# Kernel tuning notes

Hardware: AMD Instinct MI355X
Metric: run time of the kernel (lower is better)

The kernel has to match this reference:

```python
import jax, jax.numpy as jnp
import numpy as np
import math

EMBED_DIMS = 256
NUM_LANDMARKS = 40  # hard-coded k=40 in the original module
B, N = 2, 8192


def setup_inputs() -> dict:
    key = jax.random.key(0)
    ks = jax.random.split(key, 9)
    C = EMBED_DIMS
    w = lambda k: jax.random.normal(k, (C, C), dtype=jnp.float32) * 0.02
    b = lambda k: jax.random.normal(k, (C,), dtype=jnp.float32) * 0.02
    return {
        "query": jax.random.normal(ks[0], (B, N, C), dtype=jnp.float32),
        "Wq": w(ks[1]), "bq": b(ks[2]),
        "Wk": w(ks[3]), "bk": b(ks[4]),
        "Wv": w(ks[5]), "bv": b(ks[6]),
        "Wo": w(ks[7]), "bo": b(ks[8]),
    }


def reference(query, Wq, bq, Wk, bk, Wv, bv, Wo, bo):
    # key = value = identity = query (defaults in the original forward)
    C = query.shape[-1]
    scaling = math.sqrt(C)

    q = query @ Wq.T + bq  # [B, N, C]
    k = query @ Wk.T + bk
    v = query @ Wv.T + bv

    # Full similarity only to score keys: score_m[b, m] = sum_n sim_nm[b, n, m]
    sim_nm = jnp.einsum('bnc,bmc->bnm', q, k) / scaling  # [B, N, N]
    score_m = sim_nm.sum(axis=1)                          # [B, N]

    _, top_idx = jax.lax.top_k(score_m, NUM_LANDMARKS)    # [B, 40]
    selected = jnp.take_along_axis(k, top_idx[:, :, None], axis=1)  # [B, 40, C]

    sim_qn = jax.nn.softmax(jnp.einsum('bnc,bkc->bnk', q, selected) / scaling, axis=-1)  # [B, N, 40]
    sim_km = jax.nn.softmax(jnp.einsum('bmc,bkc->bmk', k, selected) / scaling, axis=-1)  # [B, N, 40]

    sim_qk = jnp.einsum('bnk,bmk->bnm', sim_qn, sim_km)   # [B, N, N]
    out = jnp.einsum('bnm,bmc->bnc', sim_qk, v)           # [B, N, C]
    out = out @ Wo.T + bo
    return query + out  # identity residual; dropouts are identity at p=0
```

## Files before the change

### kernel.cpp

```cpp
#include <hip/hip_runtime.h>
#include <cstddef>
#include <cstdint>

#define BATCH 2
#define SEQ 8192
#define CH 256
#define NLM 40
#define MROWS (BATCH * SEQ)
#define INV_SCALE 0.0625f
#define NCBLK 256

typedef unsigned short ushort_t;
typedef __attribute__((ext_vector_type(8))) short short8;
typedef __attribute__((ext_vector_type(4))) float floatx4;

__device__ __forceinline__ ushort_t f2bf(float f) {
    unsigned int u = __float_as_uint(f);
    u += 0x7FFFu + ((u >> 16) & 1u);
    return (ushort_t)(u >> 16);
}
__device__ __forceinline__ float bf2f(ushort_t u) {
    return __uint_as_float(((unsigned)u) << 16);
}

__global__ __launch_bounds__(256) void convert_colsum(const float* __restrict__ x,
                                                      ushort_t* __restrict__ xbf,
                                                      float* __restrict__ partial) {
    __shared__ float red[4][256];
    const int b = blockIdx.y;
    const int r0 = blockIdx.x * 32;
    const int t = threadIdx.x;
    const int c4 = (t & 63) * 4;
    const int rg = t >> 6;
    const float* base = x + ((size_t)b * SEQ + r0) * 256;
    ushort_t* obase = xbf + ((size_t)b * SEQ + r0) * 256;
    float4 s = {0.f, 0.f, 0.f, 0.f};
#pragma unroll
    for (int i = 0; i < 8; i++) {
        const int r = rg + i * 4;
        const float4 a = *(const float4*)&base[(size_t)r * 256 + c4];
        uint2 o;
        o.x = f2bf(a.x) | ((unsigned)f2bf(a.y) << 16);
        o.y = f2bf(a.z) | ((unsigned)f2bf(a.w) << 16);
        *(uint2*)&obase[(size_t)r * 256 + c4] = o;
        s.x += a.x; s.y += a.y; s.z += a.z; s.w += a.w;
    }
    *(float4*)&red[rg][c4] = s;
    __syncthreads();
    const float tot = red[0][t] + red[1][t] + red[2][t] + red[3][t];
    partial[((size_t)b * NCBLK + blockIdx.x) * 256 + t] = tot;
}

__global__ __launch_bounds__(256) void gemm_qkv(const ushort_t* __restrict__ xbf,
                                                const float* __restrict__ Wq,
                                                const float* __restrict__ Wk,
                                                const float* __restrict__ Wv,
                                                const float* __restrict__ bq,
                                                const float* __restrict__ bk,
                                                const float* __restrict__ bv,
                                                ushort_t* __restrict__ qkv) {
    __shared__ __align__(16) ushort_t As[128 * 72];
    __shared__ __align__(16) ushort_t Bs[64 * 40];
    const int z = blockIdx.z;
    const float* __restrict__ W = (z == 0) ? Wq : (z == 1) ? Wk : Wv;
    const float* __restrict__ bias = (z == 0) ? bq : (z == 1) ? bk : bv;
    ushort_t* __restrict__ out = qkv + (size_t)z * MROWS * 256;
    const int t = threadIdx.x;
    const int o0 = blockIdx.x * 64;
    const int m0 = blockIdx.y * 128;
    const int lane = t & 63;
    const int w = t >> 6;
    const int quad = lane >> 4;
    const int l16 = lane & 15;

    floatx4 acc[2][4];
#pragma unroll
    for (int rt = 0; rt < 2; rt++)
#pragma unroll
        for (int ct = 0; ct < 4; ct++) acc[rt][ct] = (floatx4){0.f, 0.f, 0.f, 0.f};

    for (int kc = 0; kc < 256; kc += 32) {
#pragma unroll
        for (int u = 0; u < 2; u++) {
            const int cid = t + u * 256;
            const int row = cid >> 2, off = cid & 3;
            *(uint4*)&As[row * 40 + off * 8] =
                *(const uint4*)&xbf[(size_t)(m0 + row) * 256 + kc + off * 8];
        }
        {
            const int row = t >> 2, off = t & 3;
            const float* wp = &W[(size_t)(o0 + row) * 256 + kc + off * 8];
            const float4 a = *(const float4*)wp;
            const float4 c = *(const float4*)(wp + 4);
            uint4 o;
            o.x = f2bf(a.x) | ((unsigned)f2bf(a.y) << 16);
            o.y = f2bf(a.z) | ((unsigned)f2bf(a.w) << 16);
            o.z = f2bf(c.x) | ((unsigned)f2bf(c.y) << 16);
            o.w = f2bf(c.z) | ((unsigned)f2bf(c.w) << 16);
            *(uint4*)&Bs[row * 40 + off * 8] = o;
        }
        __syncthreads();
        short8 a[2], b[4];
#pragma unroll
        for (int rt = 0; rt < 2; rt++)
            a[rt] = *(const short8*)&As[(w * 32 + rt * 16 + l16) * 40 + quad * 8];
#pragma unroll
        for (int ct = 0; ct < 4; ct++)
            b[ct] = *(const short8*)&Bs[(ct * 16 + l16) * 40 + quad * 8];
#pragma unroll
        for (int rt = 0; rt < 2; rt++)
#pragma unroll
            for (int ct = 0; ct < 4; ct++)
                acc[rt][ct] = __builtin_amdgcn_mfma_f32_16x16x32_bf16(
                    a[rt], b[ct], acc[rt][ct], 0, 0, 0);
        __syncthreads();
    }

#pragma unroll
    for (int rt = 0; rt < 2; rt++) {
#pragma unroll
        for (int ct = 0; ct < 4; ct++) {
            const int col = ct * 16 + l16;
            const float bb = bias[o0 + col];
#pragma unroll
            for (int reg = 0; reg < 4; reg++) {
                const int row = w * 32 + rt * 16 + quad * 4 + reg;
                As[row * 72 + col] = f2bf(acc[rt][ct][reg] + bb);
            }
        }
    }
    __syncthreads();
#pragma unroll
    for (int u = 0; u < 4; u++) {
        const int cid = t + u * 256;
        const int row = cid >> 3;
        const int off = (cid & 7) * 8;
        *(uint4*)&out[(size_t)(m0 + row) * 256 + o0 + off] =
            *(const uint4*)&As[row * 72 + off];
    }
}

__global__ __launch_bounds__(256) void gemm_out(const ushort_t* __restrict__ Abf,
                                                const float* __restrict__ Wo,
                                                const float* __restrict__ bias,
                                                const float* __restrict__ resid,
                                                float* __restrict__ out) {
    __shared__ __align__(16) char smem[128 * 68 * 4];
    ushort_t* As = (ushort_t*)smem;
    ushort_t* Bs = (ushort_t*)(smem + 128 * 40 * 2);
    float* Ft = (float*)smem;
    const int t = threadIdx.x;
    const int o0 = blockIdx.x * 64;
    const int m0 = blockIdx.y * 128;
    const int lane = t & 63;
    const int w = t >> 6;
    const int quad = lane >> 4;
    const int l16 = lane & 15;

    floatx4 acc[2][4];
#pragma unroll
    for (int rt = 0; rt < 2; rt++)
#pragma unroll
        for (int ct = 0; ct < 4; ct++) acc[rt][ct] = (floatx4){0.f, 0.f, 0.f, 0.f};

    for (int kc = 0; kc < 256; kc += 32) {
#pragma unroll
        for (int u = 0; u < 2; u++) {
            const int cid = t + u * 256;
            const int row = cid >> 2, off = cid & 3;
            *(uint4*)&As[row * 40 + off * 8] =
                *(const uint4*)&Abf[(size_t)(m0 + row) * 256 + kc + off * 8];
        }
        {
            const int row = t >> 2, off = t & 3;
            const float* wp = &Wo[(size_t)(o0 + row) * 256 + kc + off * 8];
            const float4 a = *(const float4*)wp;
            const float4 c = *(const float4*)(wp + 4);
            uint4 o;
            o.x = f2bf(a.x) | ((unsigned)f2bf(a.y) << 16);
            o.y = f2bf(a.z) | ((unsigned)f2bf(a.w) << 16);
            o.z = f2bf(c.x) | ((unsigned)f2bf(c.y) << 16);
            o.w = f2bf(c.z) | ((unsigned)f2bf(c.w) << 16);
            *(uint4*)&Bs[row * 40 + off * 8] = o;
        }
        __syncthreads();
        short8 a[2], b[4];
#pragma unroll
        for (int rt = 0; rt < 2; rt++)
            a[rt] = *(const short8*)&As[(w * 32 + rt * 16 + l16) * 40 + quad * 8];
#pragma unroll
        for (int ct = 0; ct < 4; ct++)
            b[ct] = *(const short8*)&Bs[(ct * 16 + l16) * 40 + quad * 8];
#pragma unroll
        for (int rt = 0; rt < 2; rt++)
#pragma unroll
            for (int ct = 0; ct < 4; ct++)
                acc[rt][ct] = __builtin_amdgcn_mfma_f32_16x16x32_bf16(
                    a[rt], b[ct], acc[rt][ct], 0, 0, 0);
        __syncthreads();
    }

#pragma unroll
    for (int rt = 0; rt < 2; rt++) {
#pragma unroll
        for (int ct = 0; ct < 4; ct++) {
            const int col = ct * 16 + l16;
            const float bb = bias[o0 + col];
#pragma unroll
            for (int reg = 0; reg < 4; reg++) {
                const int row = w * 32 + rt * 16 + quad * 4 + reg;
                Ft[row * 68 + col] = acc[rt][ct][reg] + bb;
            }
        }
    }
    __syncthreads();
#pragma unroll
    for (int u = 0; u < 8; u++) {
        const int cid = t + u * 256;
        const int row = cid >> 4;
        const int off = (cid & 15) * 4;
        const float4 v = *(const float4*)&Ft[row * 68 + off];
        const float4 r4 = *(const float4*)&resid[(size_t)(m0 + row) * 256 + o0 + off];
        float4 o;
        o.x = v.x + r4.x; o.y = v.y + r4.y; o.z = v.z + r4.z; o.w = v.w + r4.w;
        *(float4*)&out[(size_t)(m0 + row) * 256 + o0 + off] = o;
    }
}

__global__ __launch_bounds__(1024) void ws_kernel(const float* __restrict__ partial,
                                                  const float* __restrict__ Wq,
                                                  const float* __restrict__ bq,
                                                  const float* __restrict__ Wk,
                                                  float* __restrict__ ws,
                                                  float* __restrict__ tmat) {
    const int b = blockIdx.x;
    __shared__ float xs[256];
    __shared__ float qs[256];
    __shared__ float ppart[4][256];
    const int t = threadIdx.x;
    {
        float* tz = tmat + (size_t)b * NLM * 256;
        for (int i = t; i < NLM * 256; i += 1024) tz[i] = 0.f;
    }
    {
        const int c = t & 255, qd = t >> 8;
        const float* pb = partial + ((size_t)b * NCBLK + qd * 64) * 256 + c;
        float a = 0.f;
#pragma unroll 8
        for (int i = 0; i < 64; i++) a += pb[(size_t)i * 256];
        ppart[qd][c] = a;
    }
    __syncthreads();
    if (t < 256) xs[t] = ppart[0][t] + ppart[1][t] + ppart[2][t] + ppart[3][t];
    __syncthreads();
    const int lane = t & 63, w = t >> 6;
    for (int g = 0; g < 16; g++) {
        const int o = w * 16 + g;
        const float4 wq = *(const float4*)&Wq[(size_t)o * 256 + lane * 4];
        const float4 x4 = *(const float4*)&xs[lane * 4];
        float d = wq.x * x4.x + wq.y * x4.y + wq.z * x4.z + wq.w * x4.w;
#pragma unroll
        for (int off = 32; off >= 1; off >>= 1) d += __shfl_down(d, off);
        if (lane == 0) qs[o] = d + 8192.0f * bq[o];
    }
    __syncthreads();
    const int c = t & 255, part = t >> 8;
    float a = 0.f;
    for (int o = part * 64; o < part * 64 + 64; o++)
        a += Wk[(size_t)o * 256 + c] * qs[o];
    ppart[part][c] = a;
    __syncthreads();
    if (t < 256)
        ws[b * 256 + t] = ppart[0][t] + ppart[1][t] + ppart[2][t] + ppart[3][t];
}

__global__ __launch_bounds__(256) void score_kernel(const float* __restrict__ x,
                                                    const float* __restrict__ ws,
                                                    float* __restrict__ score) {
    const int b = blockIdx.y;
    const int m = blockIdx.x * 4 + (threadIdx.x >> 6);
    const int lane = threadIdx.x & 63;
    const float4 kv = *(const float4*)&x[((size_t)b * SEQ + m) * 256 + lane * 4];
    const float4 qs = *(const float4*)&ws[b * 256 + lane * 4];
    float d = kv.x * qs.x + kv.y * qs.y + kv.z * qs.z + kv.w * qs.w;
#pragma unroll
    for (int off = 32; off >= 1; off >>= 1) d += __shfl_down(d, off);
    if (lane == 0) score[(size_t)b * SEQ + m] = d * INV_SCALE;
}

__global__ __launch_bounds__(1024) void topk_gather(const float* __restrict__ score,
                                                    const ushort_t* __restrict__ kmat,
                                                    float* __restrict__ sel) {
    const int b = blockIdx.x;
    const int t = threadIdx.x;
    __shared__ unsigned hist[256];
    __shared__ unsigned wsum[64];
    __shared__ unsigned sPrefix, sMask, sRem, sNeq;
    __shared__ int sNgt;
    __shared__ int top[NLM];
    __shared__ unsigned topkey[NLM];

    unsigned key[8];
#pragma unroll
    for (int j = 0; j < 8; j++) {
        const unsigned u = __float_as_uint(score[(size_t)b * SEQ + t + j * 1024]);
        key[j] = u ^ (unsigned)(((int)u >> 31) | 0x80000000);
    }
    if (t == 0) { sPrefix = 0; sMask = 0; sRem = NLM; sNgt = 0; sNeq = 0; }

    for (int lvl = 0; lvl < 4; lvl++) {
        const int shift = 24 - 8 * lvl;
        if (t < 256) hist[t] = 0;
        __syncthreads();
        const unsigned pfx = sPrefix, msk = sMask;
#pragma unroll
        for (int j = 0; j < 8; j++)
            if (((key[j] ^ pfx) & msk) == 0)
                atomicAdd(&hist[(key[j] >> shift) & 255u], 1u);
        __syncthreads();
        if (t < 64) wsum[t] = hist[t * 4] + hist[t * 4 + 1] + hist[t * 4 + 2] + hist[t * 4 + 3];
        __syncthreads();
        if (t == 0) {
            unsigned rem = sRem, cum = 0;
            int g = 63;
            for (; g > 0; g--) { if (cum + wsum[g] >= rem) break; cum += wsum[g]; }
            int d = g * 4 + 3;
            for (; d > g * 4; d--) { if (cum + hist[d] >= rem) break; cum += hist[d]; }
            sRem = rem - cum;
            sPrefix |= ((unsigned)d) << shift;
            sMask |= 255u << shift;
        }
        __syncthreads();
    }
    const unsigned K40 = sPrefix;
    const unsigned rem = sRem;
    const int ngt = NLM - (int)rem;

#pragma unroll
    for (int j = 0; j < 8; j++) {
        if (key[j] > K40) {
            const int slot = atomicAdd(&sNgt, 1);
            top[slot] = t + j * 1024; topkey[slot] = key[j];
        } else if (key[j] == K40) {
            const unsigned e = atomicAdd(&sNeq, 1u);
            if (e < rem) {
                const int slot = ngt + (int)e;
                top[slot] = t + j * 1024; topkey[slot] = key[j];
            }
        }
    }
    __syncthreads();

    if (t < 64) {
        unsigned long long c = (t < NLM)
            ? ((((unsigned long long)(~topkey[t])) << 32) | (unsigned)top[t])
            : 0xFFFFFFFFFFFFFFFFull;
#pragma unroll
        for (int kk = 2; kk <= 64; kk <<= 1) {
#pragma unroll
            for (int j = kk >> 1; j >= 1; j >>= 1) {
                const unsigned long long o = __shfl_xor(c, j);
                const bool takeMin = ((t & kk) == 0) == ((t & j) == 0);
                const bool less = c < o;
                c = (takeMin == less) ? c : o;
            }
        }
        if (t < NLM) top[t] = (int)(c & 0xFFFFFFFFu);
    }
    __syncthreads();

    for (int f = t; f < NLM * 256; f += 1024) {
        const int j = f >> 8;
        const int cc = f & 255;
        sel[(size_t)b * NLM * 256 + f] = bf2f(kmat[((size_t)b * SEQ + top[j]) * 256 + cc]);
    }
}

__global__ __launch_bounds__(256, 4) void sim_softmax_kernel(const ushort_t* __restrict__ qbf,
                                                             const ushort_t* __restrict__ kbf,
                                                             const float* __restrict__ sel,
                                                             float* __restrict__ simq,
                                                             float* __restrict__ simk) {
    __shared__ float As_[64][68];
    __shared__ float St_[40][68];
    const int b = blockIdx.y;
    const int n0 = blockIdx.x * 64;
    const int t = threadIdx.x;
    const int r = t >> 2, c = t & 3;
    const ushort_t* __restrict__ A = (blockIdx.z == 0) ? qbf : kbf;
    float* __restrict__ sim = (blockIdx.z == 0) ? simq : simk;
    const ushort_t* __restrict__ Arow = A + ((size_t)b * SEQ + n0) * 256;
    const float* __restrict__ Sb = sel + (size_t)b * NLM * 256;

    float acc[10];
#pragma unroll
    for (int j = 0; j < 10; j++) acc[j] = 0.f;

    for (int kc = 0; kc < 256; kc += 64) {
#pragma unroll
        for (int u = 0; u < 4; u++) {
            const int f = t + u * 256;
            const int row = f >> 4;
            const int c4 = (f & 15) * 4;
            const uint2 raw = *(const uint2*)&Arow[(size_t)row * 256 + kc + c4];
            float4 fa;
            fa.x = __uint_as_float((raw.x & 0xFFFFu) << 16);
            fa.y = __uint_as_float(raw.x & 0xFFFF0000u);
            fa.z = __uint_as_float((raw.y & 0xFFFFu) << 16);
            fa.w = __uint_as_float(raw.y & 0xFFFF0000u);
            *(float4*)&As_[row][c4] = fa;
        }
#pragma unroll
        for (int u = 0; u < 3; u++) {
            const int f = t + u * 256;
            if (f < 640) {
                const int row = f >> 4;
                const int c4 = (f & 15) * 4;
                *(float4*)&St_[row][c4] = *(const float4*)&Sb[(size_t)row * 256 + kc + c4];
            }
        }
        __syncthreads();
#pragma unroll 1
        for (int i = 0; i < 64; i += 4) {
            const float4 a = *(const float4*)&As_[r][i];
#pragma unroll
            for (int j = 0; j < 10; j++) {
                const float4 s = *(const float4*)&St_[c * 10 + j][i];
                acc[j] = fmaf(a.x, s.x, acc[j]);
                acc[j] = fmaf(a.y, s.y, acc[j]);
                acc[j] = fmaf(a.z, s.z, acc[j]);
                acc[j] = fmaf(a.w, s.w, acc[j]);
            }
        }
        __syncthreads();
    }

    float mx = -1e30f;
#pragma unroll
    for (int j = 0; j < 10; j++) {
        acc[j] *= INV_SCALE;
        mx = fmaxf(mx, acc[j]);
    }
    mx = fmaxf(mx, __shfl_xor(mx, 1));
    mx = fmaxf(mx, __shfl_xor(mx, 2));
    float sum = 0.f;
#pragma unroll
    for (int j = 0; j < 10; j++) {
        acc[j] = expf(acc[j] - mx);
        sum += acc[j];
    }
    sum += __shfl_xor(sum, 1);
    sum += __shfl_xor(sum, 2);
    const float inv = 1.f / sum;
#pragma unroll
    for (int j = 0; j < 10; j++) acc[j] *= inv;

    float* __restrict__ dst = &sim[((size_t)b * SEQ + n0 + r) * NLM + c * 10];
#pragma unroll
    for (int j2 = 0; j2 < 5; j2++) {
        float2 o; o.x = acc[2 * j2]; o.y = acc[2 * j2 + 1];
        *(float2*)&dst[2 * j2] = o;
    }
}

__global__ __launch_bounds__(256) void tmat_kernel(const float* __restrict__ simk,
                                                   const ushort_t* __restrict__ v,
                                                   float* __restrict__ tmat) {
    __shared__ ushort_t Vs[64 * 256];
    __shared__ float Ps[64][40];
    const int b  = blockIdx.y;
    const int n0 = blockIdx.x * 64;
    const int t  = threadIdx.x;

#pragma unroll
    for (int u = 0; u < 8; u++) {
        const int cid = t + u * 256;
        const int row = cid >> 5, off = (cid & 31) * 8;
        *(uint4*)&Vs[row * 256 + off] =
            *(const uint4*)&v[((size_t)b * SEQ + n0 + row) * 256 + off];
    }
    float* pflat = &Ps[0][0];
    for (int f = t; f < 64 * NLM; f += 256)
        pflat[f] = simk[((size_t)b * SEQ + n0) * NLM + f];
    __syncthreads();

    float tac[40];
#pragma unroll
    for (int j = 0; j < 40; j++) tac[j] = 0.f;

#pragma unroll 2
    for (int m = 0; m < 64; m++) {
        const float vv = bf2f(Vs[m * 256 + t]);
#pragma unroll
        for (int j4 = 0; j4 < 10; j4++) {
            const float4 p = *(const float4*)&Ps[m][j4 * 4];
            tac[j4 * 4 + 0] = fmaf(p.x, vv, tac[j4 * 4 + 0]);
            tac[j4 * 4 + 1] = fmaf(p.y, vv, tac[j4 * 4 + 1]);
            tac[j4 * 4 + 2] = fmaf(p.z, vv, tac[j4 * 4 + 2]);
            tac[j4 * 4 + 3] = fmaf(p.w, vv, tac[j4 * 4 + 3]);
        }
    }
#pragma unroll
    for (int j = 0; j < 40; j++)
        atomicAdd(&tmat[(size_t)b * NLM * 256 + j * 256 + t], tac[j]);
}

__global__ __launch_bounds__(256) void out_pre_kernel(const float* __restrict__ simq,
                                                      const float* __restrict__ tmat,
                                                      ushort_t* __restrict__ outp_bf) {
    __shared__ float Pm[64][40];
    const int g0 = blockIdx.x * 64;
    const int b = g0 >> 13;
    const int t = threadIdx.x;
    float* pflat = &Pm[0][0];
    for (int f = t; f < 64 * NLM; f += 256) pflat[f] = simq[(size_t)g0 * NLM + f];
    float tc[40];
#pragma unroll
    for (int l = 0; l < 40; l++) tc[l] = tmat[(size_t)b * NLM * 256 + l * 256 + t];
    __syncthreads();
#pragma unroll 2
    for (int m = 0; m < 64; m++) {
        float a = 0.f;
#pragma unroll
        for (int j4 = 0; j4 < 10; j4++) {
            const float4 p = *(const float4*)&Pm[m][j4 * 4];
            a = fmaf(p.x, tc[j4 * 4 + 0], a);
            a = fmaf(p.y, tc[j4 * 4 + 1], a);
            a = fmaf(p.z, tc[j4 * 4 + 2], a);
            a = fmaf(p.w, tc[j4 * 4 + 3], a);
        }
        outp_bf[((size_t)g0 + m) * 256 + t] = f2bf(a);
    }
}

extern "C" void kernel_launch(void* const* d_in, const int* in_sizes, int n_in,
                              void* d_out, int out_size, void* d_ws, size_t ws_size,
                              hipStream_t stream) {
    const float* query = (const float*)d_in[0];
    const float* Wq = (const float*)d_in[1];
    const float* bq = (const float*)d_in[2];
    const float* Wk = (const float*)d_in[3];
    const float* bk = (const float*)d_in[4];
    const float* Wv = (const float*)d_in[5];
    const float* bv = (const float*)d_in[6];
    const float* Wo = (const float*)d_in[7];
    const float* bo = (const float*)d_in[8];
    float* out = (float*)d_out;

    char* p = (char*)d_ws;
    float* simq  = (float*)p;            p += (size_t)MROWS * NLM * 4;
    float* simk  = (float*)p;            p += (size_t)MROWS * NLM * 4;
    float* sel   = (float*)p;            p += (size_t)BATCH * NLM * 256 * 4;
    float* tmat  = (float*)p;            p += (size_t)BATCH * NLM * 256 * 4;
    float* partial = (float*)p;          p += (size_t)BATCH * NCBLK * 256 * 4;
    float* ws    = (float*)p;            p += (size_t)BATCH * 256 * 4;
    float* score = (float*)p;            p += (size_t)BATCH * SEQ * 4;
    ushort_t* qkv = (ushort_t*)p;        p += (size_t)3 * MROWS * 256 * 2;
    ushort_t* xbf = (ushort_t*)p;        p += (size_t)MROWS * 256 * 2;
    ushort_t* qbf = qkv;
    ushort_t* kbf = qkv + (size_t)MROWS * 256;
    ushort_t* vbf = qkv + (size_t)2 * MROWS * 256;
    ushort_t* outp_bf = xbf;

    const dim3 blk(256);

    convert_colsum<<<dim3(SEQ / 32, BATCH), blk, 0, stream>>>(query, xbf, partial);
    ws_kernel<<<dim3(BATCH), dim3(1024), 0, stream>>>(partial, Wq, bq, Wk, ws, tmat);
    score_kernel<<<dim3(SEQ / 4, BATCH), blk, 0, stream>>>(query, ws, score);

    gemm_qkv<<<dim3(4, MROWS / 128, 3), blk, 0, stream>>>(xbf, Wq, Wk, Wv, bq, bk, bv, qkv);

    topk_gather<<<dim3(BATCH), dim3(1024), 0, stream>>>(score, kbf, sel);

    sim_softmax_kernel<<<dim3(SEQ / 64, BATCH, 2), blk, 0, stream>>>(qbf, kbf, sel, simq, simk);
    tmat_kernel<<<dim3(SEQ / 64, BATCH), blk, 0, stream>>>(simk, vbf, tmat);

    out_pre_kernel<<<dim3(MROWS / 64), blk, 0, stream>>>(simq, tmat, outp_bf);
    gemm_out<<<dim3(4, MROWS / 128), blk, 0, stream>>>(outp_bf, Wo, bo, query, out);
}
```

Before: 213.2 us.

## Fuse score into QKV GEMM launch and fuse key softmax with tmat accumulation

The score dot-product kernel becomes an extra z-slice of the QKV GEMM grid, so one launch does both jobs. The key-side softmax no longer writes simk to global memory. It keeps the probabilities in shared memory, loads V tiles and accumulates tmat directly with atomics in the same block. This removes two launches and a simk write/read round trip, at the cost of more shared memory per block and imbalanced work between the z=0 and z=1 slices.

```diff
diff --git a/kernel.cpp b/kernel.cpp
--- a/kernel.cpp
+++ b/kernel.cpp
@@ -51,25 +51,93 @@
     partial[((size_t)b * NCBLK + blockIdx.x) * 256 + t] = tot;
 }
 
-__global__ __launch_bounds__(256) void gemm_qkv(const ushort_t* __restrict__ xbf,
-                                                const float* __restrict__ Wq,
-                                                const float* __restrict__ Wk,
-                                                const float* __restrict__ Wv,
-                                                const float* __restrict__ bq,
-                                                const float* __restrict__ bk,
-                                                const float* __restrict__ bv,
-                                                ushort_t* __restrict__ qkv) {
+__global__ __launch_bounds__(1024) void ws_kernel(const float* __restrict__ partial,
+                                                  const float* __restrict__ Wq,
+                                                  const float* __restrict__ bq,
+                                                  const float* __restrict__ Wk,
+                                                  float* __restrict__ ws,
+                                                  float* __restrict__ tmat) {
+    const int b = blockIdx.x;
+    __shared__ float xs[256];
+    __shared__ float qs[256];
+    __shared__ float ppart[4][256];
+    const int t = threadIdx.x;
+    {
+        float* tz = tmat + (size_t)b * NLM * 256;
+        for (int i = t; i < NLM * 256; i += 1024) tz[i] = 0.f;
+    }
+    {
+        const int c = t & 255, qd = t >> 8;
+        const float* pb = partial + ((size_t)b * NCBLK + qd * 64) * 256 + c;
+        float a = 0.f;
+#pragma unroll 8
+        for (int i = 0; i < 64; i++) a += pb[(size_t)i * 256];
+        ppart[qd][c] = a;
+    }
+    __syncthreads();
+    if (t < 256) xs[t] = ppart[0][t] + ppart[1][t] + ppart[2][t] + ppart[3][t];
+    __syncthreads();
+    const int lane = t & 63, w = t >> 6;
+    for (int g = 0; g < 16; g++) {
+        const int o = w * 16 + g;
+        const float4 wq = *(const float4*)&Wq[(size_t)o * 256 + lane * 4];
+        const float4 x4 = *(const float4*)&xs[lane * 4];
+        float d = wq.x * x4.x + wq.y * x4.y + wq.z * x4.z + wq.w * x4.w;
+#pragma unroll
+        for (int off = 32; off >= 1; off >>= 1) d += __shfl_down(d, off);
+        if (lane == 0) qs[o] = d + 8192.0f * bq[o];
+    }
+    __syncthreads();
+    const int c = t & 255, part = t >> 8;
+    float a = 0.f;
+    for (int o = part * 64; o < part * 64 + 64; o++)
+        a += Wk[(size_t)o * 256 + c] * qs[o];
+    ppart[part][c] = a;
+    __syncthreads();
+    if (t < 256)
+        ws[b * 256 + t] = ppart[0][t] + ppart[1][t] + ppart[2][t] + ppart[3][t];
+}
+
+__global__ __launch_bounds__(256) void gemm_qkv_score(const ushort_t* __restrict__ xbf,
+                                                      const float* __restrict__ Wq,
+                                                      const float* __restrict__ Wk,
+                                                      const float* __restrict__ Wv,
+                                                      const float* __restrict__ bq,
+                                                      const float* __restrict__ bk,
+                                                      const float* __restrict__ bv,
+                                                      ushort_t* __restrict__ qkv,
+                                                      const float* __restrict__ query,
+                                                      const float* __restrict__ ws,
+                                                      float* __restrict__ score) {
     __shared__ __align__(16) ushort_t As[128 * 72];
     __shared__ __align__(16) ushort_t Bs[64 * 40];
     const int z = blockIdx.z;
+    const int t = threadIdx.x;
+    const int lane = t & 63;
+    const int w = t >> 6;
+
+    if (z == 3) {
+        const int blk = blockIdx.y * 4 + blockIdx.x;
+#pragma unroll
+        for (int i = 0; i < 8; i++) {
+            const int g = blk * 32 + i * 4 + w;
+            const int b = g >> 13;
+            const int m = g & 8191;
+            const float4 kv = *(const float4*)&query[(size_t)g * 256 + lane * 4];
+            const float4 qs = *(const float4*)&ws[b * 256 + lane * 4];
+            float d = kv.x * qs.x + kv.y * qs.y + kv.z * qs.z + kv.w * qs.w;
+#pragma unroll
+            for (int off = 32; off >= 1; off >>= 1) d += __shfl_down(d, off);
+            if (lane == 0) score[(size_t)b * SEQ + m] = d * INV_SCALE;
+        }
+        return;
+    }
+
     const float* __restrict__ W = (z == 0) ? Wq : (z == 1) ? Wk : Wv;
     const float* __restrict__ bias = (z == 0) ? bq : (z == 1) ? bk : bv;
     ushort_t* __restrict__ out = qkv + (size_t)z * MROWS * 256;
-    const int t = threadIdx.x;
     const int o0 = blockIdx.x * 64;
     const int m0 = blockIdx.y * 128;
-    const int lane = t & 63;
-    const int w = t >> 6;
     const int quad = lane >> 4;
     const int l16 = lane & 15;
 
@@ -140,6 +208,246 @@
     }
 }
 
+__global__ __launch_bounds__(1024) void topk_gather(const float* __restrict__ score,
+                                                    const ushort_t* __restrict__ kmat,
+                                                    float* __restrict__ sel) {
+    const int b = blockIdx.x;
+    const int t = threadIdx.x;
+    __shared__ unsigned hist[256];
+    __shared__ unsigned wsum[64];
+    __shared__ unsigned sPrefix, sMask, sRem, sNeq;
+    __shared__ int sNgt;
+    __shared__ int top[NLM];
+    __shared__ unsigned topkey[NLM];
+
+    unsigned key[8];
+#pragma unroll
+    for (int j = 0; j < 8; j++) {
+        const unsigned u = __float_as_uint(score[(size_t)b * SEQ + t + j * 1024]);
+        key[j] = u ^ (unsigned)(((int)u >> 31) | 0x80000000);
+    }
+    if (t == 0) { sPrefix = 0; sMask = 0; sRem = NLM; sNgt = 0; sNeq = 0; }
+
+    for (int lvl = 0; lvl < 4; lvl++) {
+        const int shift = 24 - 8 * lvl;
+        if (t < 256) hist[t] = 0;
+        __syncthreads();
+        const unsigned pfx = sPrefix, msk = sMask;
+#pragma unroll
+        for (int j = 0; j < 8; j++)
+            if (((key[j] ^ pfx) & msk) == 0)
+                atomicAdd(&hist[(key[j] >> shift) & 255u], 1u);
+        __syncthreads();
+        if (t < 64) wsum[t] = hist[t * 4] + hist[t * 4 + 1] + hist[t * 4 + 2] + hist[t * 4 + 3];
+        __syncthreads();
+        if (t == 0) {
+            unsigned rem = sRem, cum = 0;
+            int g = 63;
+            for (; g > 0; g--) { if (cum + wsum[g] >= rem) break; cum += wsum[g]; }
+            int d = g * 4 + 3;
+            for (; d > g * 4; d--) { if (cum + hist[d] >= rem) break; cum += hist[d]; }
+            sRem = rem - cum;
+            sPrefix |= ((unsigned)d) << shift;
+            sMask |= 255u << shift;
+        }
+        __syncthreads();
+    }
+    const unsigned K40 = sPrefix;
+    const unsigned rem = sRem;
+    const int ngt = NLM - (int)rem;
+
+#pragma unroll
+    for (int j = 0; j < 8; j++) {
+        if (key[j] > K40) {
+            const int slot = atomicAdd(&sNgt, 1);
+            top[slot] = t + j * 1024; topkey[slot] = key[j];
+        } else if (key[j] == K40) {
+            const unsigned e = atomicAdd(&sNeq, 1u);
+            if (e < rem) {
+                const int slot = ngt + (int)e;
+                top[slot] = t + j * 1024; topkey[slot] = key[j];
+            }
+        }
+    }
+    __syncthreads();
+
+    if (t < 64) {
+        unsigned long long c = (t < NLM)
+            ? ((((unsigned long long)(~topkey[t])) << 32) | (unsigned)top[t])
+            : 0xFFFFFFFFFFFFFFFFull;
+#pragma unroll
+        for (int kk = 2; kk <= 64; kk <<= 1) {
+#pragma unroll
+            for (int j = kk >> 1; j >= 1; j >>= 1) {
+                const unsigned long long o = __shfl_xor(c, j);
+                const bool takeMin = ((t & kk) == 0) == ((t & j) == 0);
+                const bool less = c < o;
+                c = (takeMin == less) ? c : o;
+            }
+        }
+        if (t < NLM) top[t] = (int)(c & 0xFFFFFFFFu);
+    }
+    __syncthreads();
+
+    for (int f = t; f < NLM * 256; f += 1024) {
+        const int j = f >> 8;
+        const int cc = f & 255;
+        sel[(size_t)b * SEQ * 0 + (size_t)b * NLM * 256 + f] = bf2f(kmat[((size_t)b * SEQ + top[j]) * 256 + cc]);
+    }
+}
+
+__global__ __launch_bounds__(256, 4) void sim_fused(const ushort_t* __restrict__ qbf,
+                                                    const ushort_t* __restrict__ kbf,
+                                                    const ushort_t* __restrict__ vbf,
+                                                    const float* __restrict__ sel,
+                                                    float* __restrict__ simq,
+                                                    float* __restrict__ tmat) {
+    __shared__ __align__(16) char smem[43008];
+    float (*As_)[68] = (float(*)[68])smem;
+    float (*St_)[68] = (float(*)[68])(smem + 17408);
+    float (*Ps)[40]  = (float(*)[40])smem;
+    ushort_t* Vs     = (ushort_t*)(smem + 10240);
+    const int b = blockIdx.y;
+    const int n0 = blockIdx.x * 64;
+    const int t = threadIdx.x;
+    const int r = t >> 2, c = t & 3;
+    const ushort_t* __restrict__ A = (blockIdx.z == 0) ? qbf : kbf;
+    const ushort_t* __restrict__ Arow = A + ((size_t)b * SEQ + n0) * 256;
+    const float* __restrict__ Sb = sel + (size_t)b * NLM * 256;
+
+    float acc[10];
+#pragma unroll
+    for (int j = 0; j < 10; j++) acc[j] = 0.f;
+
+    for (int kc = 0; kc < 256; kc += 64) {
+#pragma unroll
+        for (int u = 0; u < 4; u++) {
+            const int f = t + u * 256;
+            const int row = f >> 4;
+            const int c4 = (f & 15) * 4;
+            const uint2 raw = *(const uint2*)&Arow[(size_t)row * 256 + kc + c4];
+            float4 fa;
+            fa.x = __uint_as_float((raw.x & 0xFFFFu) << 16);
+            fa.y = __uint_as_float(raw.x & 0xFFFF0000u);
+            fa.z = __uint_as_float((raw.y & 0xFFFFu) << 16);
+            fa.w = __uint_as_float(raw.y & 0xFFFF0000u);
+            *(float4*)&As_[row][c4] = fa;
+        }
+#pragma unroll
+        for (int u = 0; u < 3; u++) {
+            const int f = t + u * 256;
+            if (f < 640) {
+                const int row = f >> 4;
+                const int c4 = (f & 15) * 4;
+                *(float4*)&St_[row][c4] = *(const float4*)&Sb[(size_t)row * 256 + kc + c4];
+            }
+        }
+        __syncthreads();
+#pragma unroll 1
+        for (int i = 0; i < 64; i += 4) {
+            const float4 a = *(const float4*)&As_[r][i];
+#pragma unroll
+            for (int j = 0; j < 10; j++) {
+                const float4 s = *(const float4*)&St_[c * 10 + j][i];
+                acc[j] = fmaf(a.x, s.x, acc[j]);
+                acc[j] = fmaf(a.y, s.y, acc[j]);
+                acc[j] = fmaf(a.z, s.z, acc[j]);
+                acc[j] = fmaf(a.w, s.w, acc[j]);
+            }
+        }
+        __syncthreads();
+    }
+
+    float mx = -1e30f;
+#pragma unroll
+    for (int j = 0; j < 10; j++) {
+        acc[j] *= INV_SCALE;
+        mx = fmaxf(mx, acc[j]);
+    }
+    mx = fmaxf(mx, __shfl_xor(mx, 1));
+    mx = fmaxf(mx, __shfl_xor(mx, 2));
+    float sum = 0.f;
+#pragma unroll
+    for (int j = 0; j < 10; j++) {
+        acc[j] = expf(acc[j] - mx);
+        sum += acc[j];
+    }
+    sum += __shfl_xor(sum, 1);
+    sum += __shfl_xor(sum, 2);
+    const float inv = 1.f / sum;
+#pragma unroll
+    for (int j = 0; j < 10; j++) acc[j] *= inv;
+
+    if (blockIdx.z == 0) {
+        float* __restrict__ dst = &simq[((size_t)b * SEQ + n0 + r) * NLM + c * 10];
+#pragma unroll
+        for (int j2 = 0; j2 < 5; j2++) {
+            float2 o; o.x = acc[2 * j2]; o.y = acc[2 * j2 + 1];
+            *(float2*)&dst[2 * j2] = o;
+        }
+        return;
+    }
+
+#pragma unroll
+    for (int j = 0; j < 10; j++) Ps[r][c * 10 + j] = acc[j];
+#pragma unroll
+    for (int u = 0; u < 8; u++) {
+        const int cid = t + u * 256;
+        const int row = cid >> 5, off = (cid & 31) * 8;
+        *(uint4*)&Vs[row * 256 + off] =
+            *(const uint4*)&vbf[((size_t)b * SEQ + n0 + row) * 256 + off];
+    }
+    __syncthreads();
+
+    float tac[40];
+#pragma unroll
+    for (int j = 0; j < 40; j++) tac[j] = 0.f;
+
+#pragma unroll 2
+    for (int m = 0; m < 64; m++) {
+        const float vv = bf2f(Vs[m * 256 + t]);
+#pragma unroll
+        for (int j4 = 0; j4 < 10; j4++) {
+            const float4 p = *(const float4*)&Ps[m][j4 * 4];
+            tac[j4 * 4 + 0] = fmaf(p.x, vv, tac[j4 * 4 + 0]);
+            tac[j4 * 4 + 1] = fmaf(p.y, vv, tac[j4 * 4 + 1]);
+            tac[j4 * 4 + 2] = fmaf(p.z, vv, tac[j4 * 4 + 2]);
+            tac[j4 * 4 + 3] = fmaf(p.w, vv, tac[j4 * 4 + 3]);
+        }
+    }
+#pragma unroll
+    for (int j = 0; j < 40; j++)
+        atomicAdd(&tmat[(size_t)b * NLM * 256 + j * 256 + t], tac[j]);
+}
+
+__global__ __launch_bounds__(256) void out_pre_kernel(const float* __restrict__ simq,
+                                                      const float* __restrict__ tmat,
+                                                      ushort_t* __restrict__ outp_bf) {
+    __shared__ float Pm[64][40];
+    const int g0 = blockIdx.x * 64;
+    const int b = g0 >> 13;
+    const int t = threadIdx.x;
+    float* pflat = &Pm[0][0];
+    for (int f = t; f < 64 * NLM; f += 256) pflat[f] = simq[(size_t)g0 * NLM + f];
+    float tc[40];
+#pragma unroll
+    for (int l = 0; l < 40; l++) tc[l] = tmat[(size_t)b * NLM * 256 + l * 256 + t];
+    __syncthreads();
+#pragma unroll 2
+    for (int m = 0; m < 64; m++) {
+        float a = 0.f;
+#pragma unroll
+        for (int j4 = 0; j4 < 10; j4++) {
+            const float4 p = *(const float4*)&Pm[m][j4 * 4];
+            a = fmaf(p.x, tc[j4 * 4 + 0], a);
+            a = fmaf(p.y, tc[j4 * 4 + 1], a);
+            a = fmaf(p.z, tc[j4 * 4 + 2], a);
+            a = fmaf(p.w, tc[j4 * 4 + 3], a);
+        }
+        outp_bf[((size_t)g0 + m) * 256 + t] = f2bf(a);
+    }
+}
+
 __global__ __launch_bounds__(256) void gemm_out(const ushort_t* __restrict__ Abf,
                                                 const float* __restrict__ Wo,
                                                 const float* __restrict__ bias,
@@ -224,312 +532,6 @@
         float4 o;
         o.x = v.x + r4.x; o.y = v.y + r4.y; o.z = v.z + r4.z; o.w = v.w + r4.w;
         *(float4*)&out[(size_t)(m0 + row) * 256 + o0 + off] = o;
-    }
-}
-
-__global__ __launch_bounds__(1024) void ws_kernel(const float* __restrict__ partial,
-                                                  const float* __restrict__ Wq,
-                                                  const float* __restrict__ bq,
-                                                  const float* __restrict__ Wk,
-                                                  float* __restrict__ ws,
-                                                  float* __restrict__ tmat) {
-    const int b = blockIdx.x;
-    __shared__ float xs[256];
-    __shared__ float qs[256];
-    __shared__ float ppart[4][256];
-    const int t = threadIdx.x;
-    {
-        float* tz = tmat + (size_t)b * NLM * 256;
-        for (int i = t; i < NLM * 256; i += 1024) tz[i] = 0.f;
-    }
-    {
-        const int c = t & 255, qd = t >> 8;
-        const float* pb = partial + ((size_t)b * NCBLK + qd * 64) * 256 + c;
-        float a = 0.f;
-#pragma unroll 8
-        for (int i = 0; i < 64; i++) a += pb[(size_t)i * 256];
-        ppart[qd][c] = a;
-    }
-    __syncthreads();
-    if (t < 256) xs[t] = ppart[0][t] + ppart[1][t] + ppart[2][t] + ppart[3][t];
-    __syncthreads();
-    const int lane = t & 63, w = t >> 6;
-    for (int g = 0; g < 16; g++) {
-        const int o = w * 16 + g;
-        const float4 wq = *(const float4*)&Wq[(size_t)o * 256 + lane * 4];
-        const float4 x4 = *(const float4*)&xs[lane * 4];
-        float d = wq.x * x4.x + wq.y * x4.y + wq.z * x4.z + wq.w * x4.w;
-#pragma unroll
-        for (int off = 32; off >= 1; off >>= 1) d += __shfl_down(d, off);
-        if (lane == 0) qs[o] = d + 8192.0f * bq[o];
-    }
-    __syncthreads();
-    const int c = t & 255, part = t >> 8;
-    float a = 0.f;
-    for (int o = part * 64; o < part * 64 + 64; o++)
-        a += Wk[(size_t)o * 256 + c] * qs[o];
-    ppart[part][c] = a;
-    __syncthreads();
-    if (t < 256)
-        ws[b * 256 + t] = ppart[0][t] + ppart[1][t] + ppart[2][t] + ppart[3][t];
-}
-
-__global__ __launch_bounds__(256) void score_kernel(const float* __restrict__ x,
-                                                    const float* __restrict__ ws,
-                                                    float* __restrict__ score) {
-    const int b = blockIdx.y;
-    const int m = blockIdx.x * 4 + (threadIdx.x >> 6);
-    const int lane = threadIdx.x & 63;
-    const float4 kv = *(const float4*)&x[((size_t)b * SEQ + m) * 256 + lane * 4];
-    const float4 qs = *(const float4*)&ws[b * 256 + lane * 4];
-    float d = kv.x * qs.x + kv.y * qs.y + kv.z * qs.z + kv.w * qs.w;
-#pragma unroll
-    for (int off = 32; off >= 1; off >>= 1) d += __shfl_down(d, off);
-    if (lane == 0) score[(size_t)b * SEQ + m] = d * INV_SCALE;
-}
-
-__global__ __launch_bounds__(1024) void topk_gather(const float* __restrict__ score,
-                                                    const ushort_t* __restrict__ kmat,
-                                                    float* __restrict__ sel) {
-    const int b = blockIdx.x;
-    const int t = threadIdx.x;
-    __shared__ unsigned hist[256];
-    __shared__ unsigned wsum[64];
-    __shared__ unsigned sPrefix, sMask, sRem, sNeq;
-    __shared__ int sNgt;
-    __shared__ int top[NLM];
-    __shared__ unsigned topkey[NLM];
-
-    unsigned key[8];
-#pragma unroll
-    for (int j = 0; j < 8; j++) {
-        const unsigned u = __float_as_uint(score[(size_t)b * SEQ + t + j * 1024]);
-        key[j] = u ^ (unsigned)(((int)u >> 31) | 0x80000000);
-    }
-    if (t == 0) { sPrefix = 0; sMask = 0; sRem = NLM; sNgt = 0; sNeq = 0; }
-
-    for (int lvl = 0; lvl < 4; lvl++) {
-        const int shift = 24 - 8 * lvl;
-        if (t < 256) hist[t] = 0;
-        __syncthreads();
-        const unsigned pfx = sPrefix, msk = sMask;
-#pragma unroll
-        for (int j = 0; j < 8; j++)
-            if (((key[j] ^ pfx) & msk) == 0)
-                atomicAdd(&hist[(key[j] >> shift) & 255u], 1u);
-        __syncthreads();
-        if (t < 64) wsum[t] = hist[t * 4] + hist[t * 4 + 1] + hist[t * 4 + 2] + hist[t * 4 + 3];
-        __syncthreads();
-        if (t == 0) {
-            unsigned rem = sRem, cum = 0;
-            int g = 63;
-            for (; g > 0; g--) { if (cum + wsum[g] >= rem) break; cum += wsum[g]; }
-            int d = g * 4 + 3;
-            for (; d > g * 4; d--) { if (cum + hist[d] >= rem) break; cum += hist[d]; }
-            sRem = rem - cum;
-            sPrefix |= ((unsigned)d) << shift;
-            sMask |= 255u << shift;
-        }
-        __syncthreads();
-    }
-    const unsigned K40 = sPrefix;
-    const unsigned rem = sRem;
-    const int ngt = NLM - (int)rem;
-
-#pragma unroll
-    for (int j = 0; j < 8; j++) {
-        if (key[j] > K40) {
-            const int slot = atomicAdd(&sNgt, 1);
-            top[slot] = t + j * 1024; topkey[slot] = key[j];
-        } else if (key[j] == K40) {
-            const unsigned e = atomicAdd(&sNeq, 1u);
-            if (e < rem) {
-                const int slot = ngt + (int)e;
-                top[slot] = t + j * 1024; topkey[slot] = key[j];
-            }
-        }
-    }
-    __syncthreads();
-
-    if (t < 64) {
-        unsigned long long c = (t < NLM)
-            ? ((((unsigned long long)(~topkey[t])) << 32) | (unsigned)top[t])
-            : 0xFFFFFFFFFFFFFFFFull;
-#pragma unroll
-        for (int kk = 2; kk <= 64; kk <<= 1) {
-#pragma unroll
-            for (int j = kk >> 1; j >= 1; j >>= 1) {
-                const unsigned long long o = __shfl_xor(c, j);
-                const bool takeMin = ((t & kk) == 0) == ((t & j) == 0);
-                const bool less = c < o;
-                c = (takeMin == less) ? c : o;
-            }
-        }
-        if (t < NLM) top[t] = (int)(c & 0xFFFFFFFFu);
-    }
-    __syncthreads();
-
-    for (int f = t; f < NLM * 256; f += 1024) {
-        const int j = f >> 8;
-        const int cc = f & 255;
-        sel[(size_t)b * NLM * 256 + f] = bf2f(kmat[((size_t)b * SEQ + top[j]) * 256 + cc]);
-    }
-}
-
-__global__ __launch_bounds__(256, 4) void sim_softmax_kernel(const ushort_t* __restrict__ qbf,
-                                                             const ushort_t* __restrict__ kbf,
-                                                             const float* __restrict__ sel,
-                                                             float* __restrict__ simq,
-                                                             float* __restrict__ simk) {
-    __shared__ float As_[64][68];
-    __shared__ float St_[40][68];
-    const int b = blockIdx.y;
-    const int n0 = blockIdx.x * 64;
-    const int t = threadIdx.x;
-    const int r = t >> 2, c = t & 3;
-    const ushort_t* __restrict__ A = (blockIdx.z == 0) ? qbf : kbf;
-    float* __restrict__ sim = (blockIdx.z == 0) ? simq : simk;
-    const ushort_t* __restrict__ Arow = A + ((size_t)b * SEQ + n0) * 256;
-    const float* __restrict__ Sb = sel + (size_t)b * NLM * 256;
-
-    float acc[10];
-#pragma unroll
-    for (int j = 0; j < 10; j++) acc[j] = 0.f;
-
-    for (int kc = 0; kc < 256; kc += 64) {
-#pragma unroll
-        for (int u = 0; u < 4; u++) {
-            const int f = t + u * 256;
-            const int row = f >> 4;
-            const int c4 = (f & 15) * 4;
-            const uint2 raw = *(const uint2*)&Arow[(size_t)row * 256 + kc + c4];
-            float4 fa;
-            fa.x = __uint_as_float((raw.x & 0xFFFFu) << 16);
-            fa.y = __uint_as_float(raw.x & 0xFFFF0000u);
-            fa.z = __uint_as_float((raw.y & 0xFFFFu) << 16);
-            fa.w = __uint_as_float(raw.y & 0xFFFF0000u);
-            *(float4*)&As_[row][c4] = fa;
-        }
-#pragma unroll
-        for (int u = 0; u < 3; u++) {
-            const int f = t + u * 256;
-            if (f < 640) {
-                const int row = f >> 4;
-                const int c4 = (f & 15) * 4;
-                *(float4*)&St_[row][c4] = *(const float4*)&Sb[(size_t)row * 256 + kc + c4];
-            }
-        }
-        __syncthreads();
-#pragma unroll 1
-        for (int i = 0; i < 64; i += 4) {
-            const float4 a = *(const float4*)&As_[r][i];
-#pragma unroll
-            for (int j = 0; j < 10; j++) {
-                const float4 s = *(const float4*)&St_[c * 10 + j][i];
-                acc[j] = fmaf(a.x, s.x, acc[j]);
-                acc[j] = fmaf(a.y, s.y, acc[j]);
-                acc[j] = fmaf(a.z, s.z, acc[j]);
-                acc[j] = fmaf(a.w, s.w, acc[j]);
-            }
-        }
-        __syncthreads();
-    }
-
-    float mx = -1e30f;
-#pragma unroll
-    for (int j = 0; j < 10; j++) {
-        acc[j] *= INV_SCALE;
-        mx = fmaxf(mx, acc[j]);
-    }
-    mx = fmaxf(mx, __shfl_xor(mx, 1));
-    mx = fmaxf(mx, __shfl_xor(mx, 2));
-    float sum = 0.f;
-#pragma unroll
-    for (int j = 0; j < 10; j++) {
-        acc[j] = expf(acc[j] - mx);
-        sum += acc[j];
-    }
-    sum += __shfl_xor(sum, 1);
-    sum += __shfl_xor(sum, 2);
-    const float inv = 1.f / sum;
-#pragma unroll
-    for (int j = 0; j < 10; j++) acc[j] *= inv;
-
-    float* __restrict__ dst = &sim[((size_t)b * SEQ + n0 + r) * NLM + c * 10];
-#pragma unroll
-    for (int j2 = 0; j2 < 5; j2++) {
-        float2 o; o.x = acc[2 * j2]; o.y = acc[2 * j2 + 1];
-        *(float2*)&dst[2 * j2] = o;
-    }
-}
-
-__global__ __launch_bounds__(256) void tmat_kernel(const float* __restrict__ simk,
-                                                   const ushort_t* __restrict__ v,
-                                                   float* __restrict__ tmat) {
-    __shared__ ushort_t Vs[64 * 256];
-    __shared__ float Ps[64][40];
-    const int b  = blockIdx.y;
-    const int n0 = blockIdx.x * 64;
-    const int t  = threadIdx.x;
-
-#pragma unroll
-    for (int u = 0; u < 8; u++) {
-        const int cid = t + u * 256;
-        const int row = cid >> 5, off = (cid & 31) * 8;
-        *(uint4*)&Vs[row * 256 + off] =
-            *(const uint4*)&v[((size_t)b * SEQ + n0 + row) * 256 + off];
-    }
-    float* pflat = &Ps[0][0];
-    for (int f = t; f < 64 * NLM; f += 256)
-        pflat[f] = simk[((size_t)b * SEQ + n0) * NLM + f];
-    __syncthreads();
-
-    float tac[40];
-#pragma unroll
-    for (int j = 0; j < 40; j++) tac[j] = 0.f;
-
-#pragma unroll 2
-    for (int m = 0; m < 64; m++) {
-        const float vv = bf2f(Vs[m * 256 + t]);
-#pragma unroll
-        for (int j4 = 0; j4 < 10; j4++) {
-            const float4 p = *(const float4*)&Ps[m][j4 * 4];
-            tac[j4 * 4 + 0] = fmaf(p.x, vv, tac[j4 * 4 + 0]);
-            tac[j4 * 4 + 1] = fmaf(p.y, vv, tac[j4 * 4 + 1]);
-            tac[j4 * 4 + 2] = fmaf(p.z, vv, tac[j4 * 4 + 2]);
-            tac[j4 * 4 + 3] = fmaf(p.w, vv, tac[j4 * 4 + 3]);
-        }
-    }
-#pragma unroll
-    for (int j = 0; j < 40; j++)
-        atomicAdd(&tmat[(size_t)b * NLM * 256 + j * 256 + t], tac[j]);
-}
-
-__global__ __launch_bounds__(256) void out_pre_kernel(const float* __restrict__ simq,
-                                                      const float* __restrict__ tmat,
-                                                      ushort_t* __restrict__ outp_bf) {
-    __shared__ float Pm[64][40];
-    const int g0 = blockIdx.x * 64;
-    const int b = g0 >> 13;
-    const int t = threadIdx.x;
-    float* pflat = &Pm[0][0];
-    for (int f = t; f < 64 * NLM; f += 256) pflat[f] = simq[(size_t)g0 * NLM + f];
-    float tc[40];
-#pragma unroll
-    for (int l = 0; l < 40; l++) tc[l] = tmat[(size_t)b * NLM * 256 + l * 256 + t];
-    __syncthreads();
-#pragma unroll 2
-    for (int m = 0; m < 64; m++) {
-        float a = 0.f;
-#pragma unroll
-        for (int j4 = 0; j4 < 10; j4++) {
-            const float4 p = *(const float4*)&Pm[m][j4 * 4];
-            a = fmaf(p.x, tc[j4 * 4 + 0], a);
-            a = fmaf(p.y, tc[j4 * 4 + 1], a);
-            a = fmaf(p.z, tc[j4 * 4 + 2], a);
-            a = fmaf(p.w, tc[j4 * 4 + 3], a);
-        }
-        outp_bf[((size_t)g0 + m) * 256 + t] = f2bf(a);
     }
 }
 
@@ -549,7 +551,6 @@
 
     char* p = (char*)d_ws;
     float* simq  = (float*)p;            p += (size_t)MROWS * NLM * 4;
-    float* simk  = (float*)p;            p += (size_t)MROWS * NLM * 4;
     float* sel   = (float*)p;            p += (size_t)BATCH * NLM * 256 * 4;
     float* tmat  = (float*)p;            p += (size_t)BATCH * NLM * 256 * 4;
     float* partial = (float*)p;          p += (size_t)BATCH * NCBLK * 256 * 4;
@@ -566,14 +567,13 @@
 
     convert_colsum<<<dim3(SEQ / 32, BATCH), blk, 0, stream>>>(query, xbf, partial);
     ws_kernel<<<dim3(BATCH), dim3(1024), 0, stream>>>(partial, Wq, bq, Wk, ws, tmat);
-    score_kernel<<<dim3(SEQ / 4, BATCH), blk, 0, stream>>>(query, ws, score);
-
-    gemm_qkv<<<dim3(4, MROWS / 128, 3), blk, 0, stream>>>(xbf, Wq, Wk, Wv, bq, bk, bv, qkv);
+
+    gemm_qkv_score<<<dim3(4, MROWS / 128, 4), blk, 0, stream>>>(
+        xbf, Wq, Wk, Wv, bq, bk, bv, qkv, query, ws, score);
 
     topk_gather<<<dim3(BATCH), dim3(1024), 0, stream>>>(score, kbf, sel);
 
-    sim_softmax_kernel<<<dim3(SEQ / 64, BATCH, 2), blk, 0, stream>>>(qbf, kbf, sel, simq, simk);
-    tmat_kernel<<<dim3(SEQ / 64, BATCH), blk, 0, stream>>>(simk, vbf, tmat);
+    sim_fused<<<dim3(SEQ / 64, BATCH, 2), blk, 0, stream>>>(qbf, kbf, vbf, sel, simq, tmat);
 
     out_pre_kernel<<<dim3(MROWS / 64), blk, 0, stream>>>(simq, tmat, outp_bf);
     gemm_out<<<dim3(4, MROWS / 128), blk, 0, stream>>>(outp_bf, Wo, bo, query, out);
```

Result: faster. 204.7 us (-4.0%).
